# Optimization experiments

Hardware: AMD Instinct MI355X
Metric: run time of the kernel (lower is better)

The kernel has to match this reference:

```python
import jax, jax.numpy as jnp
import numpy as np

NEG_SLOPE = 0.2


def gat_conv(x, src, dst, W, att_src, att_dst, bias, heads, out_ch, concat):
    """PyG-style GATConv (eval mode, self-loops already appended to src/dst)."""
    N = x.shape[0]
    h = (x @ W).reshape(N, heads, out_ch)                      # [N,H,C]
    a_src = jnp.einsum('nhc,hc->nh', h, att_src)               # [N,H]
    a_dst = jnp.einsum('nhc,hc->nh', h, att_dst)               # [N,H]
    e = jax.nn.leaky_relu(a_src[src] + a_dst[dst], NEG_SLOPE)  # [E,H]
    # numerically-stable softmax segmented by destination node
    emax = jax.ops.segment_max(e, dst, num_segments=N)         # [N,H]
    e = jnp.exp(e - emax[dst])
    denom = jax.ops.segment_sum(e, dst, num_segments=N)
    alpha = e / (denom[dst] + 1e-16)                           # [E,H]
    msg = h[src] * alpha[..., None]                            # [E,H,C]
    out = jax.ops.segment_sum(msg, dst, num_segments=N)        # [N,H,C]
    out = out.reshape(N, heads * out_ch) if concat else out.mean(axis=1)
    return out + bias


def setup_inputs() -> dict:
    key = jax.random.key(0)
    ks = jax.random.split(key, 9)
    N, E, IN, OUT = 100000, 1600000, 128, 40
    H1, C1 = 8, 8
    x = jax.random.normal(ks[0], (N, IN), dtype=jnp.float32)
    edge_index = jax.random.randint(ks[1], (2, E), 0, N, dtype=jnp.int64)
    s = 0.1
    return {
        'x': x,
        'edge_index': edge_index,
        'W1': jax.random.normal(ks[2], (IN, H1 * C1), dtype=jnp.float32) * s,
        'att_src1': jax.random.normal(ks[3], (H1, C1), dtype=jnp.float32) * s,
        'att_dst1': jax.random.normal(ks[4], (H1, C1), dtype=jnp.float32) * s,
        'b1': jnp.zeros((H1 * C1,), dtype=jnp.float32),
        'W2': jax.random.normal(ks[5], (H1 * C1, OUT), dtype=jnp.float32) * s,
        'att_src2': jax.random.normal(ks[6], (1, OUT), dtype=jnp.float32) * s,
        'att_dst2': jax.random.normal(ks[7], (1, OUT), dtype=jnp.float32) * s,
        'b2': jnp.zeros((OUT,), dtype=jnp.float32),
    }


def reference(x, edge_index, W1, att_src1, att_dst1, b1, W2, att_src2, att_dst2, b2):
    N = x.shape[0]
    loops = jnp.arange(N, dtype=edge_index.dtype)
    src = jnp.concatenate([edge_index[0], loops])  # self-loops (PyG default)
    dst = jnp.concatenate([edge_index[1], loops])
    h = gat_conv(x, src, dst, W1, att_src1, att_dst1, b1, 8, 8, True)
    h = jax.nn.elu(h)  # dropout is identity in eval mode
    out = gat_conv(h, src, dst, W2, att_src2, att_dst2, b2, 1, W2.shape[1], False)
    return jax.nn.log_softmax(out, axis=-1)
```

## Files before the change

### kernel.cpp

```cpp
#include <hip/hip_runtime.h>
#include <math.h>

#define NEG_SLOPE 0.2f
#define BSHIFT 8
#define MAXBUK 512

typedef __attribute__((ext_vector_type(8))) short short8;
typedef __attribute__((ext_vector_type(4))) float floatx4;

static __device__ __forceinline__ float lrelu_exp(float e) {
    e = fmaxf(e, NEG_SLOPE * e);
    return __expf(e);
}

static __device__ __forceinline__ short f2bf(float f) {
    union { float f; unsigned u; } v; v.f = f;
    unsigned r = v.u + 0x7FFFu + ((v.u >> 16) & 1u);
    return (short)(r >> 16);
}
static __device__ __forceinline__ float bf2f(unsigned short s) {
    union { float f; unsigned u; } v;
    v.u = ((unsigned)s) << 16;
    return v.f;
}
static __device__ __forceinline__ float bfpair_lo(unsigned v) {
    union { float f; unsigned u; } x; x.u = v << 16; return x.f;
}
static __device__ __forceinline__ float bfpair_hi(unsigned v) {
    union { float f; unsigned u; } x; x.u = v & 0xffff0000u; return x.f;
}
static __device__ __forceinline__ void splitbf(float f, short& hi, short& lo) {
    hi = f2bf(f);
    lo = f2bf(f - bf2f((unsigned short)hi));
}


__global__ __launch_bounds__(512) void k_hist(const int* __restrict__ dst, int E, int CHUNK,
                                              int NBLK, int NBUK, int* __restrict__ blockhist) {
    __shared__ int hist[MAXBUK];
    int t = threadIdx.x, b = blockIdx.x;
    for (int i = t; i < NBUK; i += 512) hist[i] = 0;
    __syncthreads();
    int e0 = b * CHUNK, e1 = e0 + CHUNK; if (e1 > E) e1 = E;
    for (int e = e0 + t; e < e1; e += 512) atomicAdd(&hist[dst[e] >> BSHIFT], 1);
    __syncthreads();
    for (int i = t; i < NBUK; i += 512) blockhist[(size_t)i * NBLK + b] = hist[i];
}

__global__ __launch_bounds__(256) void k_colscan(int* __restrict__ blockhist,
                                                 int* __restrict__ btot, int NBLK) {
    int bucket = blockIdx.x, t = threadIdx.x;
    int lane = t & 63, wv = t >> 6;
    __shared__ int wsum[4];
    __shared__ int carry_s;
    if (t == 0) carry_s = 0;
    __syncthreads();
    for (int base = 0; base < NBLK; base += 256) {
        int idx = base + t;
        int v = (idx < NBLK) ? blockhist[(size_t)bucket * NBLK + idx] : 0;
        int s = v;
#pragma unroll
        for (int o = 1; o < 64; o <<= 1) {
            int u = __shfl_up(s, o, 64);
            if (lane >= o) s += u;
        }
        if (lane == 63) wsum[wv] = s;
        __syncthreads();
        int b0 = 0;
#pragma unroll
        for (int w = 0; w < 4; ++w) b0 += (w < wv) ? wsum[w] : 0;
        int excl = s + b0 - v + carry_s;
        if (idx < NBLK) blockhist[(size_t)bucket * NBLK + idx] = excl;
        __syncthreads();
        if (t == 255) carry_s += s + b0;
        __syncthreads();
    }
    if (t == 0) btot[bucket] = carry_s;
}

__global__ __launch_bounds__(512) void k_bucket_scan(const int* __restrict__ btot,
                                                     int* __restrict__ bucketbase, int NBUK) {
    __shared__ int sh[512];
    int t = threadIdx.x;
    int v = (t < NBUK) ? btot[t] : 0;
    sh[t] = v;
    __syncthreads();
#pragma unroll
    for (int o = 1; o < 512; o <<= 1) {
        int u = (t >= o) ? sh[t - o] : 0;
        __syncthreads();
        sh[t] += u;
        __syncthreads();
    }
    if (t < NBUK) bucketbase[t] = sh[t] - v;
    if (t == NBUK - 1) bucketbase[NBUK] = sh[t];
}

__global__ __launch_bounds__(512) void k_partition(const int* __restrict__ src,
                                                   const int* __restrict__ dst, int E, int CHUNK,
                                                   int NBLK, int NBUK,
                                                   const int* __restrict__ blockhist,
                                                   const int* __restrict__ bucketbase,
                                                   unsigned* __restrict__ packed) {
    __shared__ int cur[MAXBUK];
    int t = threadIdx.x, b = blockIdx.x;
    for (int i = t; i < NBUK; i += 512)
        cur[i] = blockhist[(size_t)i * NBLK + b] + bucketbase[i];
    __syncthreads();
    int e0 = b * CHUNK, e1 = e0 + CHUNK; if (e1 > E) e1 = E;
    for (int e = e0 + t; e < e1; e += 512) {
        int d = dst[e], s = src[e];
        int pos = atomicAdd(&cur[d >> BSHIFT], 1);
        packed[pos] = ((unsigned)s << 8) | ((unsigned)d & 255u);
    }
}

__global__ __launch_bounds__(256) void k_fine(const unsigned* __restrict__ packed,
                                              const int* __restrict__ bucketbase,
                                              int* __restrict__ offsets,
                                              int* __restrict__ csr_src,
                                              int N, int NBUK) {
    __shared__ int fcnt[256];
    __shared__ int wsum[4];
    int bucket = blockIdx.x, t = threadIdx.x;
    int lo = bucket << BSHIFT;
    int nn = N - lo; if (nn > 256) nn = 256;
    int ebase = bucketbase[bucket];
    int ecnt = bucketbase[bucket + 1] - ebase;
    fcnt[t] = 0;
    __syncthreads();
    for (int i = t; i < ecnt; i += 256) {
        unsigned p = packed[ebase + i];
        atomicAdd(&fcnt[p & 255u], 1);
    }
    __syncthreads();
    int v = fcnt[t];
    int lane = t & 63, wv = t >> 6;
    int s = v;
#pragma unroll
    for (int o = 1; o < 64; o <<= 1) {
        int u = __shfl_up(s, o, 64);
        if (lane >= o) s += u;
    }
    if (lane == 63) wsum[wv] = s;
    __syncthreads();
    int base = 0;
#pragma unroll
    for (int w = 0; w < 4; ++w) base += (w < wv) ? wsum[w] : 0;
    int excl = s + base - v;
    if (t < nn) offsets[lo + t] = ebase + excl;
    if (bucket == NBUK - 1 && t == 0) offsets[N] = ebase + ecnt;
    __syncthreads();
    fcnt[t] = excl;
    __syncthreads();
    for (int i = t; i < ecnt; i += 256) {
        unsigned p = packed[ebase + i];
        int pos = atomicAdd(&fcnt[p & 255u], 1);
        csr_src[ebase + pos] = (int)(p >> 8);
    }
}

__global__ __launch_bounds__(256) void k_splitW2(const float* __restrict__ W2,
                                                 short* __restrict__ w2h,
                                                 short* __restrict__ w2l) {
    int i = blockIdx.x * 256 + threadIdx.x;
    if (i < 64 * 48) {
        int row = i / 48, col = i % 48;
        short hi = 0, lo = 0;
        if (col < 40) splitbf(W2[row * 40 + col], hi, lo);
        w2h[i] = hi; w2l[i] = lo;
    }
}

__global__ __launch_bounds__(256) void k_gemm1(const float* __restrict__ x,
                                               const float* __restrict__ W1,
                                               const float* __restrict__ att_s,
                                               const float* __restrict__ att_d,
                                               unsigned short* __restrict__ h1b,
                                               float* __restrict__ a_s1,
                                               float* __restrict__ a_d1, int N) {
    int tid = threadIdx.x, wave = tid >> 6, lane = tid & 63;
    int n16 = lane & 15, q = lane >> 4;
    int nb = blockIdx.x * 64 + wave * 16;
    if (nb >= N) return;

    short8 bfr[4][4];
#pragma unroll
    for (int ct = 0; ct < 4; ++ct) {
        int n = ct * 16 + n16;
#pragma unroll
        for (int kc = 0; kc < 4; ++kc) {
            int k0 = kc * 32 + q * 8;
            short8 b;
#pragma unroll
            for (int j = 0; j < 8; ++j) b[j] = f2bf(W1[(k0 + j) * 64 + n]);
            bfr[ct][kc] = b;
        }
    }

    int arow = nb + n16; if (arow >= N) arow = N - 1;
    const float* xr = x + (size_t)arow * 128 + q * 8;
    short8 afr[4];
#pragma unroll
    for (int kc = 0; kc < 4; ++kc) {
        float4 u0 = *(const float4*)(xr + kc * 32);
        float4 u1 = *(const float4*)(xr + kc * 32 + 4);
        short8 a;
        a[0] = f2bf(u0.x); a[1] = f2bf(u0.y); a[2] = f2bf(u0.z); a[3] = f2bf(u0.w);
        a[4] = f2bf(u1.x); a[5] = f2bf(u1.y); a[6] = f2bf(u1.z); a[7] = f2bf(u1.w);
        afr[kc] = a;
    }

    floatx4 acc[4];
#pragma unroll
    for (int ct = 0; ct < 4; ++ct) {
        floatx4 c = {0.f, 0.f, 0.f, 0.f};
#pragma unroll
        for (int kc = 0; kc < 4; ++kc)
            c = __builtin_amdgcn_mfma_f32_16x16x32_bf16(afr[kc], bfr[ct][kc], c, 0, 0, 0);
        acc[ct] = c;
    }

#pragma unroll
    for (int ct = 0; ct < 4; ++ct) {
#pragma unroll
        for (int r = 0; r < 4; ++r) {
            int row = nb + q * 4 + r;
            if (row < N) h1b[(size_t)row * 64 + ct * 16 + n16] = (unsigned short)f2bf(acc[ct][r]);
        }
    }

#pragma unroll
    for (int ct = 0; ct < 4; ++ct) {
        float as = att_s[ct * 16 + n16];
        float ad = att_d[ct * 16 + n16];
#pragma unroll
        for (int r = 0; r < 4; ++r) {
            float ps = acc[ct][r] * as;
            float pd = acc[ct][r] * ad;
#pragma unroll
            for (int m = 1; m < 8; m <<= 1) {
                ps += __shfl_xor(ps, m, 64);
                pd += __shfl_xor(pd, m, 64);
            }
            int row = nb + q * 4 + r;
            if ((n16 & 7) == 0 && row < N) {
                int h = 2 * ct + (n16 >> 3);
                a_s1[row * 8 + h] = ps;
                a_d1[row * 8 + h] = pd;
            }
        }
    }
}

__global__ __launch_bounds__(256) void k_agg1(const unsigned short* __restrict__ h1b,
                                              const float* __restrict__ a_s1,
                                              const float* __restrict__ a_d1,
                                              const int* __restrict__ offsets,
                                              const int* __restrict__ csr_src,
                                              const float* __restrict__ b1,
                                              float* __restrict__ y1, int N) {
    int wave = threadIdx.x >> 6, lane = threadIdx.x & 63;
    int d = blockIdx.x * 4 + wave;
    if (d >= N) return;
    int g = lane >> 3;
    int h = lane & 7;
    float ad = a_d1[d * 8 + h];
    float acc[8] = {0.f, 0.f, 0.f, 0.f, 0.f, 0.f, 0.f, 0.f};
    float wsum_l = 0.f;
    if (g == 0) {
        float w0 = lrelu_exp(a_s1[d * 8 + h] + ad);
        uint4 v = *(const uint4*)(h1b + (size_t)d * 64 + 8 * h);
        acc[0] = w0 * bfpair_lo(v.x); acc[1] = w0 * bfpair_hi(v.x);
        acc[2] = w0 * bfpair_lo(v.y); acc[3] = w0 * bfpair_hi(v.y);
        acc[4] = w0 * bfpair_lo(v.z); acc[5] = w0 * bfpair_hi(v.z);
        acc[6] = w0 * bfpair_lo(v.w); acc[7] = w0 * bfpair_hi(v.w);
        wsum_l = w0;
    }
    int i0 = offsets[d], i1 = offsets[d + 1];
    for (int base = i0; base < i1; base += 64) {
        int m = i1 - base; if (m > 64) m = 64;
        int sv = (lane < m) ? csr_src[base + lane] : 0;
        for (int j = 0; j < m; j += 16) {
            int eA = j + g;
            int siA = __shfl(sv, eA, 64);
            bool liveB = (j + 8 < m);
            if (liveB) {
                int eB = j + 8 + g;
                int siB = __shfl(sv, eB, 64);
                float evA = a_s1[siA * 8 + h] + ad;
                float evB = a_s1[siB * 8 + h] + ad;
                uint4 vA = *(const uint4*)(h1b + (size_t)siA * 64 + 8 * h);
                uint4 vB = *(const uint4*)(h1b + (size_t)siB * 64 + 8 * h);
                float wA = (eA < m) ? lrelu_exp(evA) : 0.f;
                float wB = (eB < m) ? lrelu_exp(evB) : 0.f;
                wsum_l += wA + wB;
                acc[0] = fmaf(wA, bfpair_lo(vA.x), acc[0]);
                acc[1] = fmaf(wA, bfpair_hi(vA.x), acc[1]);
                acc[2] = fmaf(wA, bfpair_lo(vA.y), acc[2]);
                acc[3] = fmaf(wA, bfpair_hi(vA.y), acc[3]);
                acc[4] = fmaf(wA, bfpair_lo(vA.z), acc[4]);
                acc[5] = fmaf(wA, bfpair_hi(vA.z), acc[5]);
                acc[6] = fmaf(wA, bfpair_lo(vA.w), acc[6]);
                acc[7] = fmaf(wA, bfpair_hi(vA.w), acc[7]);
                acc[0] = fmaf(wB, bfpair_lo(vB.x), acc[0]);
                acc[1] = fmaf(wB, bfpair_hi(vB.x), acc[1]);
                acc[2] = fmaf(wB, bfpair_lo(vB.y), acc[2]);
                acc[3] = fmaf(wB, bfpair_hi(vB.y), acc[3]);
                acc[4] = fmaf(wB, bfpair_lo(vB.z), acc[4]);
                acc[5] = fmaf(wB, bfpair_hi(vB.z), acc[5]);
                acc[6] = fmaf(wB, bfpair_lo(vB.w), acc[6]);
                acc[7] = fmaf(wB, bfpair_hi(vB.w), acc[7]);
            } else {
                float evA = a_s1[siA * 8 + h] + ad;
                uint4 vA = *(const uint4*)(h1b + (size_t)siA * 64 + 8 * h);
                float wA = (eA < m) ? lrelu_exp(evA) : 0.f;
                wsum_l += wA;
                acc[0] = fmaf(wA, bfpair_lo(vA.x), acc[0]);
                acc[1] = fmaf(wA, bfpair_hi(vA.x), acc[1]);
                acc[2] = fmaf(wA, bfpair_lo(vA.y), acc[2]);
                acc[3] = fmaf(wA, bfpair_hi(vA.y), acc[3]);
                acc[4] = fmaf(wA, bfpair_lo(vA.z), acc[4]);
                acc[5] = fmaf(wA, bfpair_hi(vA.z), acc[5]);
                acc[6] = fmaf(wA, bfpair_lo(vA.w), acc[6]);
                acc[7] = fmaf(wA, bfpair_hi(vA.w), acc[7]);
            }
        }
    }
#pragma unroll
    for (int mm = 8; mm < 64; mm <<= 1) {
#pragma unroll
        for (int k = 0; k < 8; ++k) acc[k] += __shfl_xor(acc[k], mm, 64);
        wsum_l += __shfl_xor(wsum_l, mm, 64);
    }
    if (g == 0) {
        float inv = 1.f / (wsum_l + 1e-16f);
        float4 bA = *(const float4*)(b1 + 8 * h);
        float4 bB = *(const float4*)(b1 + 8 * h + 4);
        float o[8];
        o[0] = acc[0] * inv + bA.x;
        o[1] = acc[1] * inv + bA.y;
        o[2] = acc[2] * inv + bA.z;
        o[3] = acc[3] * inv + bA.w;
        o[4] = acc[4] * inv + bB.x;
        o[5] = acc[5] * inv + bB.y;
        o[6] = acc[6] * inv + bB.z;
        o[7] = acc[7] * inv + bB.w;
#pragma unroll
        for (int k = 0; k < 8; ++k) o[k] = o[k] > 0.f ? o[k] : (__expf(o[k]) - 1.f);
        float4 s0 = make_float4(o[0], o[1], o[2], o[3]);
        float4 s1 = make_float4(o[4], o[5], o[6], o[7]);
        *(float4*)(y1 + (size_t)d * 64 + 8 * h) = s0;
        *(float4*)(y1 + (size_t)d * 64 + 8 * h + 4) = s1;
    }
}

__global__ __launch_bounds__(256) void k_gemm2(const float* __restrict__ y1,
                                               const short* __restrict__ w2h,
                                               const short* __restrict__ w2l,
                                               const float* __restrict__ att_s,
                                               const float* __restrict__ att_d,
                                               unsigned short* __restrict__ h2b,
                                               float* __restrict__ a2s,
                                               float* __restrict__ a2d, int N) {
    int tid = threadIdx.x, wave = tid >> 6, lane = tid & 63;
    int n16 = lane & 15, q = lane >> 4;
    int nb = blockIdx.x * 64 + wave * 16;
    if (nb >= N) return;

    int arow = nb + n16; if (arow >= N) arow = N - 1;
    const float* yr = y1 + (size_t)arow * 64 + q * 8;
    short8 ah[2], al[2];
#pragma unroll
    for (int kc = 0; kc < 2; ++kc) {
        float4 u0 = *(const float4*)(yr + kc * 32);
        float4 u1 = *(const float4*)(yr + kc * 32 + 4);
        short8 h, l; short hi, lo;
        splitbf(u0.x, hi, lo); h[0] = hi; l[0] = lo;
        splitbf(u0.y, hi, lo); h[1] = hi; l[1] = lo;
        splitbf(u0.z, hi, lo); h[2] = hi; l[2] = lo;
        splitbf(u0.w, hi, lo); h[3] = hi; l[3] = lo;
        splitbf(u1.x, hi, lo); h[4] = hi; l[4] = lo;
        splitbf(u1.y, hi, lo); h[5] = hi; l[5] = lo;
        splitbf(u1.z, hi, lo); h[6] = hi; l[6] = lo;
        splitbf(u1.w, hi, lo); h[7] = hi; l[7] = lo;
        ah[kc] = h; al[kc] = l;
    }

    float psr[4] = {0.f, 0.f, 0.f, 0.f}, pdr[4] = {0.f, 0.f, 0.f, 0.f};
#pragma unroll
    for (int ct = 0; ct < 3; ++ct) {
        int n = ct * 16 + n16;
        short8 bh0, bh1, bl0, bl1;
#pragma unroll
        for (int j = 0; j < 8; ++j) {
            int k0 = q * 8 + j;
            bh0[j] = w2h[k0 * 48 + n];
            bl0[j] = w2l[k0 * 48 + n];
            bh1[j] = w2h[(32 + k0) * 48 + n];
            bl1[j] = w2l[(32 + k0) * 48 + n];
        }
        floatx4 c = {0.f, 0.f, 0.f, 0.f};
        c = __builtin_amdgcn_mfma_f32_16x16x32_bf16(ah[0], bl0, c, 0, 0, 0);
        c = __builtin_amdgcn_mfma_f32_16x16x32_bf16(al[0], bh0, c, 0, 0, 0);
        c = __builtin_amdgcn_mfma_f32_16x16x32_bf16(ah[0], bh0, c, 0, 0, 0);
        c = __builtin_amdgcn_mfma_f32_16x16x32_bf16(ah[1], bl1, c, 0, 0, 0);
        c = __builtin_amdgcn_mfma_f32_16x16x32_bf16(al[1], bh1, c, 0, 0, 0);
        c = __builtin_amdgcn_mfma_f32_16x16x32_bf16(ah[1], bh1, c, 0, 0, 0);

        int col = ct * 16 + n16;
#pragma unroll
        for (int r = 0; r < 4; ++r) {
            int row = nb + q * 4 + r;
            if (col < 40 && row < N) h2b[(size_t)row * 40 + col] = (unsigned short)f2bf(c[r]);
        }
        float asv = (col < 40) ? att_s[col] : 0.f;
        float adv = (col < 40) ? att_d[col] : 0.f;
#pragma unroll
        for (int r = 0; r < 4; ++r) {
            psr[r] = fmaf(c[r], asv, psr[r]);
            pdr[r] = fmaf(c[r], adv, pdr[r]);
        }
    }
#pragma unroll
    for (int r = 0; r < 4; ++r) {
        float ps = psr[r], pd = pdr[r];
#pragma unroll
        for (int m = 1; m < 16; m <<= 1) {
            ps += __shfl_xor(ps, m, 64);
            pd += __shfl_xor(pd, m, 64);
        }
        int row = nb + q * 4 + r;
        if (n16 == 0 && row < N) { a2s[row] = ps; a2d[row] = pd; }
    }
}

__global__ __launch_bounds__(256) void k_agg2(const unsigned short* __restrict__ h2b,
                                              const float* __restrict__ a2s,
                                              const float* __restrict__ a2d,
                                              const int* __restrict__ offsets,
                                              const int* __restrict__ csr_src,
                                              const float* __restrict__ b2,
                                              float* __restrict__ out, int N) {
    int wave = threadIdx.x >> 6, lane = threadIdx.x & 63;
    int d = blockIdx.x * 4 + wave;
    if (d >= N) return;
    bool act = (lane < 60);
    int g = act ? (lane / 5) : 0;
    int c = act ? (lane - g * 5) : 0;
    float ad = a2d[d];
    float w0 = lrelu_exp(a2s[d] + ad);
    float acc[8] = {0.f, 0.f, 0.f, 0.f, 0.f, 0.f, 0.f, 0.f};
    if (lane < 5) {
        uint4 v = *(const uint4*)(h2b + (size_t)d * 40 + 8 * c);
        acc[0] = w0 * bfpair_lo(v.x); acc[1] = w0 * bfpair_hi(v.x);
        acc[2] = w0 * bfpair_lo(v.y); acc[3] = w0 * bfpair_hi(v.y);
        acc[4] = w0 * bfpair_lo(v.z); acc[5] = w0 * bfpair_hi(v.z);
        acc[6] = w0 * bfpair_lo(v.w); acc[7] = w0 * bfpair_hi(v.w);
    }
    float wsum_l = 0.f;
    int i0 = offsets[d], i1 = offsets[d + 1];
    for (int base = i0; base < i1; base += 60) {
        int m = i1 - base; if (m > 60) m = 60;
        int sv = 0; float wv = 0.f;
        if (lane < m) {
            sv = csr_src[base + lane];
            wv = lrelu_exp(a2s[sv] + ad);
        }
        wsum_l += wv;
        for (int j = 0; j < m; j += 24) {
            int eA = j + g;
            int siA = __shfl(sv, eA, 64);
            float wqA = __shfl(wv, eA, 64);
            if (!act || eA >= m) wqA = 0.f;
            bool liveB = (j + 12 < m);
            if (liveB) {
                int eB = j + 12 + g;
                int siB = __shfl(sv, eB, 64);
                float wqB = __shfl(wv, eB, 64);
                if (!act || eB >= m) wqB = 0.f;
                uint4 vA = *(const uint4*)(h2b + (size_t)siA * 40 + 8 * c);
                uint4 vB = *(const uint4*)(h2b + (size_t)siB * 40 + 8 * c);
                acc[0] = fmaf(wqA, bfpair_lo(vA.x), acc[0]);
                acc[1] = fmaf(wqA, bfpair_hi(vA.x), acc[1]);
                acc[2] = fmaf(wqA, bfpair_lo(vA.y), acc[2]);
                acc[3] = fmaf(wqA, bfpair_hi(vA.y), acc[3]);
                acc[4] = fmaf(wqA, bfpair_lo(vA.z), acc[4]);
                acc[5] = fmaf(wqA, bfpair_hi(vA.z), acc[5]);
                acc[6] = fmaf(wqA, bfpair_lo(vA.w), acc[6]);
                acc[7] = fmaf(wqA, bfpair_hi(vA.w), acc[7]);
                acc[0] = fmaf(wqB, bfpair_lo(vB.x), acc[0]);
                acc[1] = fmaf(wqB, bfpair_hi(vB.x), acc[1]);
                acc[2] = fmaf(wqB, bfpair_lo(vB.y), acc[2]);
                acc[3] = fmaf(wqB, bfpair_hi(vB.y), acc[3]);
                acc[4] = fmaf(wqB, bfpair_lo(vB.z), acc[4]);
                acc[5] = fmaf(wqB, bfpair_hi(vB.z), acc[5]);
                acc[6] = fmaf(wqB, bfpair_lo(vB.w), acc[6]);
                acc[7] = fmaf(wqB, bfpair_hi(vB.w), acc[7]);
            } else {
                uint4 vA = *(const uint4*)(h2b + (size_t)siA * 40 + 8 * c);
                acc[0] = fmaf(wqA, bfpair_lo(vA.x), acc[0]);
                acc[1] = fmaf(wqA, bfpair_hi(vA.x), acc[1]);
                acc[2] = fmaf(wqA, bfpair_lo(vA.y), acc[2]);
                acc[3] = fmaf(wqA, bfpair_hi(vA.y), acc[3]);
                acc[4] = fmaf(wqA, bfpair_lo(vA.z), acc[4]);
                acc[5] = fmaf(wqA, bfpair_hi(vA.z), acc[5]);
                acc[6] = fmaf(wqA, bfpair_lo(vA.w), acc[6]);
                acc[7] = fmaf(wqA, bfpair_hi(vA.w), acc[7]);
            }
        }
    }
#pragma unroll
    for (int k = 0; k < 8; ++k) {
        acc[k] += __shfl(acc[k], lane + 30, 64);
        acc[k] += __shfl(acc[k], lane + 15, 64);
        acc[k] += __shfl(acc[k], lane + 5, 64) + __shfl(acc[k], lane + 10, 64);
    }
#pragma unroll
    for (int mm = 1; mm < 64; mm <<= 1) wsum_l += __shfl_xor(wsum_l, mm, 64);
    float wsum = wsum_l + w0;
    bool act5 = (lane < 5);
    float inv = 1.f / (wsum + 1e-16f);
    float o[8];
    float4 bA = *(const float4*)(b2 + 8 * c);
    float4 bB = *(const float4*)(b2 + 8 * c + 4);
    o[0] = acc[0] * inv + bA.x;
    o[1] = acc[1] * inv + bA.y;
    o[2] = acc[2] * inv + bA.z;
    o[3] = acc[3] * inv + bA.w;
    o[4] = acc[4] * inv + bB.x;
    o[5] = acc[5] * inv + bB.y;
    o[6] = acc[6] * inv + bB.z;
    o[7] = acc[7] * inv + bB.w;
    float mxl = -INFINITY;
    if (act5) {
        mxl = fmaxf(fmaxf(fmaxf(o[0], o[1]), fmaxf(o[2], o[3])),
                    fmaxf(fmaxf(o[4], o[5]), fmaxf(o[6], o[7])));
    }
#pragma unroll
    for (int mm = 1; mm < 8; mm <<= 1) mxl = fmaxf(mxl, __shfl_xor(mxl, mm, 64));
    float exl = 0.f;
    if (act5) {
#pragma unroll
        for (int k = 0; k < 8; ++k) exl += __expf(o[k] - mxl);
    }
#pragma unroll
    for (int mm = 1; mm < 8; mm <<= 1) exl += __shfl_xor(exl, mm, 64);
    if (act5) {
        float lse = mxl + __logf(exl);
        float4 s0 = make_float4(o[0] - lse, o[1] - lse, o[2] - lse, o[3] - lse);
        float4 s1 = make_float4(o[4] - lse, o[5] - lse, o[6] - lse, o[7] - lse);
        *(float4*)(out + (size_t)d * 40 + 8 * c) = s0;
        *(float4*)(out + (size_t)d * 40 + 8 * c + 4) = s1;
    }
}


extern "C" void kernel_launch(void* const* d_in, const int* in_sizes, int n_in,
                              void* d_out, int out_size, void* d_ws, size_t ws_size,
                              hipStream_t stream) {
    const float* x   = (const float*)d_in[0];
    const int*   ei  = (const int*)d_in[1];
    const float* W1  = (const float*)d_in[2];
    const float* as1 = (const float*)d_in[3];
    const float* ad1 = (const float*)d_in[4];
    const float* b1  = (const float*)d_in[5];
    const float* W2  = (const float*)d_in[6];
    const float* as2 = (const float*)d_in[7];
    const float* ad2 = (const float*)d_in[8];
    const float* b2  = (const float*)d_in[9];
    float* out = (float*)d_out;

    int N = in_sizes[0] / 128;
    int E = in_sizes[1] / 2;
    const int* src = ei;
    const int* dst = ei + E;

    int NBUK = (N + 255) >> BSHIFT;
    int CHUNK = 4096;
    int NBLK = (E + CHUNK - 1) / CHUNK;

    char* ws = (char*)d_ws;
    size_t off = 0;
    auto alloc = [&](size_t bytes) -> char* {
        char* p = ws + off;
        off += (bytes + 255) & ~(size_t)255;
        return p;
    };
    unsigned short* h1b = (unsigned short*)alloc((size_t)N * 64 * 2);
    float* a_s1    = (float*)alloc((size_t)N * 8 * 4);
    float* a_d1    = (float*)alloc((size_t)N * 8 * 4);
    float* y1      = (float*)alloc((size_t)N * 64 * 4);
    size_t shared_sz = (size_t)N * 40 * 2;
    if ((size_t)E * 4 > shared_sz) shared_sz = (size_t)E * 4;
    char*  region  = alloc(shared_sz);
    unsigned short* h2b = (unsigned short*)region;
    unsigned* packed    = (unsigned*)region;
    float* a2s     = (float*)alloc((size_t)N * 4);
    float* a2d     = (float*)alloc((size_t)N * 4);
    int*   offsets = (int*)alloc((size_t)(N + 1) * 4);
    int*   csr_src = (int*)alloc((size_t)E * 4);
    int*   blockhist  = (int*)alloc((size_t)NBUK * NBLK * 4);
    int*   btot       = (int*)alloc((size_t)NBUK * 4);
    int*   bucketbase = (int*)alloc((size_t)(NBUK + 1) * 4);
    short* w2h     = (short*)alloc((size_t)64 * 48 * 2);
    short* w2l     = (short*)alloc((size_t)64 * 48 * 2);

    int nb = (N + 3) / 4;
    int gb = (N + 63) / 64;

    k_hist<<<NBLK, 512, 0, stream>>>(dst, E, CHUNK, NBLK, NBUK, blockhist);
    k_colscan<<<NBUK, 256, 0, stream>>>(blockhist, btot, NBLK);
    k_bucket_scan<<<1, 512, 0, stream>>>(btot, bucketbase, NBUK);
    k_partition<<<NBLK, 512, 0, stream>>>(src, dst, E, CHUNK, NBLK, NBUK, blockhist,
                                          bucketbase, packed);
    k_fine<<<NBUK, 256, 0, stream>>>(packed, bucketbase, offsets, csr_src, N, NBUK);
    k_splitW2<<<12, 256, 0, stream>>>(W2, w2h, w2l);
    k_gemm1<<<gb, 256, 0, stream>>>(x, W1, as1, ad1, h1b, a_s1, a_d1, N);
    k_agg1<<<nb, 256, 0, stream>>>(h1b, a_s1, a_d1, offsets, csr_src, b1, y1, N);
    k_gemm2<<<gb, 256, 0, stream>>>(y1, w2h, w2l, as2, ad2, h2b, a2s, a2d, N);
    k_agg2<<<nb, 256, 0, stream>>>(h2b, a2s, a2d, offsets, csr_src, b2, out, N);
}
```

Measured before the change: 192.7 us.

## Process four destination nodes per wave in layer-2 aggregation

Restructures k_agg2 so each 16-lane quarter of a wave handles its own destination node, instead of one node per full wave. With average degree around 16, the old mapping left most of the 60 lanes idle. The new mapping has each lane load its edge source index and exponent directly, with no shuffle staging, and needs fewer reduction shuffles. The cost is that each quarter loops to the wave's maximum degree, which adds divergence when degrees differ, and only 15 of 16 lanes do useful work.

```diff
diff --git a/kernel.cpp b/kernel.cpp
--- a/kernel.cpp
+++ b/kernel.cpp
@@ -443,87 +443,73 @@
                                               const float* __restrict__ b2,
                                               float* __restrict__ out, int N) {
     int wave = threadIdx.x >> 6, lane = threadIdx.x & 63;
-    int d = blockIdx.x * 4 + wave;
-    if (d >= N) return;
-    bool act = (lane < 60);
-    int g = act ? (lane / 5) : 0;
-    int c = act ? (lane - g * 5) : 0;
-    float ad = a2d[d];
-    float w0 = lrelu_exp(a2s[d] + ad);
+    int q = lane >> 4;
+    int ll = lane & 15;
+    int d = (blockIdx.x * 4 + wave) * 4 + q;
+    bool dvalid = (d < N);
+    int de = dvalid ? d : N - 1;
+    int g = ll / 5;
+    int c = ll - g * 5;
+    bool lane_ok = (ll < 15);
+    float ad = a2d[de];
+    float w0 = lrelu_exp(a2s[de] + ad);
+    int i0 = offsets[de];
+    int deg = offsets[de + 1] - i0;
+    if (!dvalid) deg = 0;
+    int dmax = deg;
+    dmax = max(dmax, __shfl_xor(dmax, 16, 64));
+    dmax = max(dmax, __shfl_xor(dmax, 32, 64));
     float acc[8] = {0.f, 0.f, 0.f, 0.f, 0.f, 0.f, 0.f, 0.f};
-    if (lane < 5) {
-        uint4 v = *(const uint4*)(h2b + (size_t)d * 40 + 8 * c);
+    float wsum_l = 0.f;
+    if (g == 0) {
+        uint4 v = *(const uint4*)(h2b + (size_t)de * 40 + 8 * c);
         acc[0] = w0 * bfpair_lo(v.x); acc[1] = w0 * bfpair_hi(v.x);
         acc[2] = w0 * bfpair_lo(v.y); acc[3] = w0 * bfpair_hi(v.y);
         acc[4] = w0 * bfpair_lo(v.z); acc[5] = w0 * bfpair_hi(v.z);
         acc[6] = w0 * bfpair_lo(v.w); acc[7] = w0 * bfpair_hi(v.w);
     }
-    float wsum_l = 0.f;
-    int i0 = offsets[d], i1 = offsets[d + 1];
-    for (int base = i0; base < i1; base += 60) {
-        int m = i1 - base; if (m > 60) m = 60;
-        int sv = 0; float wv = 0.f;
-        if (lane < m) {
-            sv = csr_src[base + lane];
-            wv = lrelu_exp(a2s[sv] + ad);
-        }
-        wsum_l += wv;
-        for (int j = 0; j < m; j += 24) {
-            int eA = j + g;
-            int siA = __shfl(sv, eA, 64);
-            float wqA = __shfl(wv, eA, 64);
-            if (!act || eA >= m) wqA = 0.f;
-            bool liveB = (j + 12 < m);
-            if (liveB) {
-                int eB = j + 12 + g;
-                int siB = __shfl(sv, eB, 64);
-                float wqB = __shfl(wv, eB, 64);
-                if (!act || eB >= m) wqB = 0.f;
-                uint4 vA = *(const uint4*)(h2b + (size_t)siA * 40 + 8 * c);
-                uint4 vB = *(const uint4*)(h2b + (size_t)siB * 40 + 8 * c);
-                acc[0] = fmaf(wqA, bfpair_lo(vA.x), acc[0]);
-                acc[1] = fmaf(wqA, bfpair_hi(vA.x), acc[1]);
-                acc[2] = fmaf(wqA, bfpair_lo(vA.y), acc[2]);
-                acc[3] = fmaf(wqA, bfpair_hi(vA.y), acc[3]);
-                acc[4] = fmaf(wqA, bfpair_lo(vA.z), acc[4]);
-                acc[5] = fmaf(wqA, bfpair_hi(vA.z), acc[5]);
-                acc[6] = fmaf(wqA, bfpair_lo(vA.w), acc[6]);
-                acc[7] = fmaf(wqA, bfpair_hi(vA.w), acc[7]);
-                acc[0] = fmaf(wqB, bfpair_lo(vB.x), acc[0]);
-                acc[1] = fmaf(wqB, bfpair_hi(vB.x), acc[1]);
-                acc[2] = fmaf(wqB, bfpair_lo(vB.y), acc[2]);
-                acc[3] = fmaf(wqB, bfpair_hi(vB.y), acc[3]);
-                acc[4] = fmaf(wqB, bfpair_lo(vB.z), acc[4]);
-                acc[5] = fmaf(wqB, bfpair_hi(vB.z), acc[5]);
-                acc[6] = fmaf(wqB, bfpair_lo(vB.w), acc[6]);
-                acc[7] = fmaf(wqB, bfpair_hi(vB.w), acc[7]);
-            } else {
-                uint4 vA = *(const uint4*)(h2b + (size_t)siA * 40 + 8 * c);
-                acc[0] = fmaf(wqA, bfpair_lo(vA.x), acc[0]);
-                acc[1] = fmaf(wqA, bfpair_hi(vA.x), acc[1]);
-                acc[2] = fmaf(wqA, bfpair_lo(vA.y), acc[2]);
-                acc[3] = fmaf(wqA, bfpair_hi(vA.y), acc[3]);
-                acc[4] = fmaf(wqA, bfpair_lo(vA.z), acc[4]);
-                acc[5] = fmaf(wqA, bfpair_hi(vA.z), acc[5]);
-                acc[6] = fmaf(wqA, bfpair_lo(vA.w), acc[6]);
-                acc[7] = fmaf(wqA, bfpair_hi(vA.w), acc[7]);
-            }
-        }
-    }
-#pragma unroll
-    for (int k = 0; k < 8; ++k) {
-        acc[k] += __shfl(acc[k], lane + 30, 64);
-        acc[k] += __shfl(acc[k], lane + 15, 64);
+    for (int j = 0; j < dmax; j += 6) {
+        int jA = j + g, jB = j + 3 + g;
+        bool liveA = lane_ok && (jA < deg);
+        bool liveB = lane_ok && (jB < deg);
+        int svA = de, svB = de;
+        if (liveA) svA = csr_src[i0 + jA];
+        if (liveB) svB = csr_src[i0 + jB];
+        float eA = a2s[svA] + ad;
+        float eB = a2s[svB] + ad;
+        uint4 vA = *(const uint4*)(h2b + (size_t)svA * 40 + 8 * c);
+        uint4 vB = *(const uint4*)(h2b + (size_t)svB * 40 + 8 * c);
+        float wA = liveA ? lrelu_exp(eA) : 0.f;
+        float wB = liveB ? lrelu_exp(eB) : 0.f;
+        if (c == 0) wsum_l += wA + wB;
+        acc[0] = fmaf(wA, bfpair_lo(vA.x), acc[0]);
+        acc[1] = fmaf(wA, bfpair_hi(vA.x), acc[1]);
+        acc[2] = fmaf(wA, bfpair_lo(vA.y), acc[2]);
+        acc[3] = fmaf(wA, bfpair_hi(vA.y), acc[3]);
+        acc[4] = fmaf(wA, bfpair_lo(vA.z), acc[4]);
+        acc[5] = fmaf(wA, bfpair_hi(vA.z), acc[5]);
+        acc[6] = fmaf(wA, bfpair_lo(vA.w), acc[6]);
+        acc[7] = fmaf(wA, bfpair_hi(vA.w), acc[7]);
+        acc[0] = fmaf(wB, bfpair_lo(vB.x), acc[0]);
+        acc[1] = fmaf(wB, bfpair_hi(vB.x), acc[1]);
+        acc[2] = fmaf(wB, bfpair_lo(vB.y), acc[2]);
+        acc[3] = fmaf(wB, bfpair_hi(vB.y), acc[3]);
+        acc[4] = fmaf(wB, bfpair_lo(vB.z), acc[4]);
+        acc[5] = fmaf(wB, bfpair_hi(vB.z), acc[5]);
+        acc[6] = fmaf(wB, bfpair_lo(vB.w), acc[6]);
+        acc[7] = fmaf(wB, bfpair_hi(vB.w), acc[7]);
+    }
+#pragma unroll
+    for (int k = 0; k < 8; ++k)
         acc[k] += __shfl(acc[k], lane + 5, 64) + __shfl(acc[k], lane + 10, 64);
-    }
-#pragma unroll
-    for (int mm = 1; mm < 64; mm <<= 1) wsum_l += __shfl_xor(wsum_l, mm, 64);
+    wsum_l += __shfl(wsum_l, lane + 5, 64) + __shfl(wsum_l, lane + 10, 64);
+    wsum_l = __shfl(wsum_l, lane & 48, 64);
     float wsum = wsum_l + w0;
-    bool act5 = (lane < 5);
+    bool act5 = (ll < 5) && dvalid;
     float inv = 1.f / (wsum + 1e-16f);
-    float o[8];
     float4 bA = *(const float4*)(b2 + 8 * c);
     float4 bB = *(const float4*)(b2 + 8 * c + 4);
+    float o[8];
     o[0] = acc[0] * inv + bA.x;
     o[1] = acc[1] * inv + bA.y;
     o[2] = acc[2] * inv + bA.z;
@@ -607,6 +593,7 @@
     short* w2l     = (short*)alloc((size_t)64 * 48 * 2);
 
     int nb = (N + 3) / 4;
+    int nb2 = (N + 15) / 16;
     int gb = (N + 63) / 64;
 
     k_hist<<<NBLK, 512, 0, stream>>>(dst, E, CHUNK, NBLK, NBUK, blockhist);
@@ -619,5 +606,5 @@
     k_gemm1<<<gb, 256, 0, stream>>>(x, W1, as1, ad1, h1b, a_s1, a_d1, N);
     k_agg1<<<nb, 256, 0, stream>>>(h1b, a_s1, a_d1, offsets, csr_src, b1, y1, N);
     k_gemm2<<<gb, 256, 0, stream>>>(y1, w2h, w2l, as2, ad2, h2b, a2s, a2d, N);
-    k_agg2<<<nb, 256, 0, stream>>>(h2b, a2s, a2d, offsets, csr_src, b2, out, N);
-}
+    k_agg2<<<nb2, 256, 0, stream>>>(h2b, a2s, a2d, offsets, csr_src, b2, out, N);
+}
```

After: 172.6 us. 1.12x faster.
